# Kernel tuning notes

Measured on AMD Instinct MI355X. Metric: run time of the kernel, lower is better.

Reference implementation:

```python
import jax, jax.numpy as jnp
import numpy as np

N_NODES = 50000
N_EDGES = 800000
HID = 128


def setup_inputs() -> dict:
    key = jax.random.key(0)
    ks = jax.random.split(key, 10)
    s_msg = 1.0 / np.sqrt(2 * HID + 1)
    s_u1 = 1.0 / np.sqrt(2 * HID)
    s_u2 = 1.0 / np.sqrt(HID)
    return {
        "z": jax.random.normal(ks[0], (N_NODES, HID), dtype=jnp.float32),
        "edge_weight": jax.random.uniform(ks[1], (N_EDGES,), dtype=jnp.float32),
        "edge_src": jax.random.randint(ks[2], (N_EDGES,), 0, N_NODES),
        "edge_dst": jax.random.randint(ks[3], (N_EDGES,), 0, N_NODES),
        "Wm": jax.random.normal(ks[4], (2 * HID + 1, HID), dtype=jnp.float32) * s_msg,
        "bm": jax.random.normal(ks[5], (HID,), dtype=jnp.float32) * s_msg,
        "W1": jax.random.normal(ks[6], (2 * HID, HID), dtype=jnp.float32) * s_u1,
        "b1": jax.random.normal(ks[7], (HID,), dtype=jnp.float32) * s_u1,
        "W2": jax.random.normal(ks[8], (HID, HID), dtype=jnp.float32) * s_u2,
        "b2": jax.random.normal(ks[9], (HID,), dtype=jnp.float32) * s_u2,
    }


def reference(z, edge_weight, edge_src, edge_dst, Wm, bm, W1, b1, W2, b2):
    n, H = z.shape
    # message Linear on concat([z[u], z[v], w]) split to avoid materializing [E, 2H+1]
    Wd, Ws, ww = Wm[:H], Wm[H:2 * H], Wm[2 * H]  # [H,H], [H,H], [H]
    msgs = (z[edge_dst] @ Wd + z[edge_src] @ Ws
            + edge_weight[:, None] * ww[None, :] + bm)  # [E, H]
    # max-aggregate messages per destination node; zeros for isolated nodes
    agg = jax.ops.segment_max(msgs, edge_dst, num_segments=n)  # [n, H], -inf if empty
    deg = jax.ops.segment_sum(jnp.ones_like(edge_weight), edge_dst, num_segments=n)
    agg = jnp.where(deg[:, None] > 0, agg, jnp.zeros((), dtype=z.dtype))
    # update MLP on concat([z, agg]) split into two GEMMs
    W1a, W1b = W1[:H], W1[H:]
    hidden = jax.nn.relu(z @ W1a + agg @ W1b + b1)  # [n, H]
    return hidden @ W2 + b2  # [n, H]
```

## Files before the change

kernel.cpp:

```cpp
#include <hip/hip_runtime.h>
#include <hip/hip_bf16.h>

#define HID 128

typedef short bf16x8 __attribute__((ext_vector_type(8)));
typedef float f32x4  __attribute__((ext_vector_type(4)));
typedef unsigned short u16;
typedef unsigned long long u64;

__device__ __forceinline__ u16 f2bf(float f) {
    __hip_bfloat16 h = __float2bfloat16(f);
    return *reinterpret_cast<u16*>(&h);
}
__device__ __forceinline__ float bf2f(u16 x) {
    unsigned u = ((unsigned)x) << 16;
    return __uint_as_float(u);
}
__device__ __forceinline__ u64 pack_rec(int dst, int src, float w) {
    int wq = (int)fmaf(w, 32768.f, 0.5f);
    wq = wq > 32767 ? 32767 : wq;
    return ((u64)(unsigned)dst << 31) | ((unsigned)src << 15) | (unsigned)wq;
}


__global__ __launch_bounds__(256)
void hist_kernel(const int* __restrict__ edst, int* __restrict__ bhist,
                 int E, int nbk)
{
    __shared__ int lh[256];
    const int b = blockIdx.x;
    const int t = threadIdx.x;
    lh[t] = 0;
    __syncthreads();
    const int e0 = b * 4096;
    const int eend = min(e0 + 4096, E);
    for (int e = e0 + t; e < eend; e += 256)
        atomicAdd(&lh[edst[e] >> 8], 1);
    __syncthreads();
    if (t < nbk && lh[t] > 0) atomicAdd(&bhist[t], lh[t]);
}

__global__ __launch_bounds__(256)
void cast_scatter(const float* __restrict__ z, const float* __restrict__ Wm,
                  const float* __restrict__ W1, const float* __restrict__ W2,
                  const int* __restrict__ esrc, const int* __restrict__ edst,
                  const float* __restrict__ ew,
                  const int* __restrict__ bhist, int* __restrict__ brun,
                  u16* __restrict__ Ab, u16* __restrict__ Wt, u64* __restrict__ tmp,
                  int N, int Mp, int E, int bz, int bw, int nbk)
{
    const int b = blockIdx.x;
    const int t = threadIdx.x;
    if (b < bz) {
        const int idx8 = (b * 256 + t) * 8;
        const int row = idx8 >> 7, col = idx8 & 127;
        bf16x8 u;
        if (row < N) {
            const float4 v0 = *(const float4*)&z[(size_t)row * 128 + col];
            const float4 v1 = *(const float4*)&z[(size_t)row * 128 + col + 4];
            u[0] = (short)f2bf(v0.x); u[1] = (short)f2bf(v0.y);
            u[2] = (short)f2bf(v0.z); u[3] = (short)f2bf(v0.w);
            u[4] = (short)f2bf(v1.x); u[5] = (short)f2bf(v1.y);
            u[6] = (short)f2bf(v1.z); u[7] = (short)f2bf(v1.w);
        } else { u = bf16x8{0,0,0,0,0,0,0,0}; }
        *(bf16x8*)&Ab[(size_t)row * 256 + col] = u;
    } else if (b < bz + bw) {
        const int idx = (b - bz) * 256 + t;
        float v;
        if (idx < 32768) {
            const int nn = idx >> 7, k = idx & 127;
            v = (nn < 128) ? Wm[k * 128 + nn] : Wm[(128 + k) * 128 + (nn - 128)];
        } else if (idx < 65536) {
            const int j = idx - 32768, n = j >> 8, k = j & 255;
            v = W1[k * 128 + n];
        } else {
            const int j = idx - 65536, n = j >> 7, k = j & 127;
            v = W2[k * 128 + n];
        }
        Wt[idx] = f2bf(v);
    } else {
        __shared__ int cnt[256];
        __shared__ int rbase[256];
        __shared__ int bbase[256];
        __shared__ int ps[256];
        const int e0 = (b - bz - bw) * 4096;
        const int eend = min(e0 + 4096, E);

        const int h = (t < nbk) ? bhist[t] : 0;
        ps[t] = h;
        __syncthreads();
        for (int off = 1; off < 256; off <<= 1) {
            int add = (t >= off) ? ps[t - off] : 0;
            __syncthreads();
            ps[t] += add;
            __syncthreads();
        }
        bbase[t] = ps[t] - h;
        cnt[t] = 0;
        __syncthreads();

        if (eend - e0 == 4096) {
            int myb[16]; u64 myrec[16];
#pragma unroll
            for (int i = 0; i < 16; i++) {
                const int e = e0 + t + i * 256;
                const int d = edst[e];
                myb[i] = d >> 8;
                myrec[i] = pack_rec(d, esrc[e], ew[e]);
                atomicAdd(&cnt[myb[i]], 1);
            }
            __syncthreads();
            if (t < nbk && cnt[t] > 0) rbase[t] = bbase[t] + atomicAdd(&brun[t], cnt[t]);
            __syncthreads();
            cnt[t] = 0;
            __syncthreads();
#pragma unroll
            for (int i = 0; i < 16; i++) {
                const int r = atomicAdd(&cnt[myb[i]], 1);
                tmp[(size_t)rbase[myb[i]] + r] = myrec[i];
            }
        } else {
            for (int e = e0 + t; e < eend; e += 256)
                atomicAdd(&cnt[edst[e] >> 8], 1);
            __syncthreads();
            if (t < nbk && cnt[t] > 0) rbase[t] = bbase[t] + atomicAdd(&brun[t], cnt[t]);
            __syncthreads();
            cnt[t] = 0;
            __syncthreads();
            for (int e = e0 + t; e < eend; e += 256) {
                const int d = edst[e];
                const int bk = d >> 8;
                const int r = atomicAdd(&cnt[bk], 1);
                tmp[(size_t)rbase[bk] + r] = pack_rec(d, esrc[e], ew[e]);
            }
        }
    }
}

__global__ __launch_bounds__(256)
void sort_gemmP(const u64* __restrict__ tmp, const int* __restrict__ bhist,
                int* __restrict__ offsets, unsigned* __restrict__ s_ew,
                int N, int E, int nbk,
                const u16* __restrict__ Ab, const u16* __restrict__ Wt,
                u16* __restrict__ Pb, int Mp, int nP,
                const float* __restrict__ Wm, const float* __restrict__ b1,
                const float* __restrict__ bm,
                u16* __restrict__ W1f, float* __restrict__ bprime)
{
    const int t = threadIdx.x;

    if (blockIdx.x < (unsigned)nbk) {
        __shared__ int cnt[256];
        __shared__ int cur[256];
        __shared__ int ps[256];
        const int b = blockIdx.x;
        const int n0 = b << 8;
        const int nhi = min(256, N - n0);

        const int h = (t < nbk) ? bhist[t] : 0;
        ps[t] = h;
        __syncthreads();
        for (int off = 1; off < 256; off <<= 1) {
            int add = (t >= off) ? ps[t - off] : 0;
            __syncthreads();
            ps[t] += add;
            __syncthreads();
        }
        const int base = (b > 0) ? ps[b - 1] : 0;
        const int endp = ps[b];
        cnt[t] = 0;
        __syncthreads();

        for (int r = base + t; r < endp; r += 256)
            atomicAdd(&cnt[(int)(tmp[r] >> 31) - n0], 1);
        __syncthreads();

        const int v = cnt[t];
        ps[t] = v;
        __syncthreads();
        for (int off = 1; off < 256; off <<= 1) {
            int add = (t >= off) ? ps[t - off] : 0;
            __syncthreads();
            ps[t] += add;
            __syncthreads();
        }
        cur[t] = base + ps[t] - v;
        __syncthreads();

        if (t < nhi) offsets[n0 + t] = cur[t];
        if (t == 0 && n0 + nhi == N) offsets[N] = E;

        for (int r = base + t; r < endp; r += 256) {
            const u64 rec = tmp[r];
            const int local = (int)(rec >> 31) - n0;
            const int pos = atomicAdd(&cur[local], 1);
            s_ew[pos] = (unsigned)(rec & 0x7FFFFFFFu);
        }
    } else if (blockIdx.x < (unsigned)(nbk + nP)) {
        __shared__ u16 As[64 * 136];
        const int row0 = (blockIdx.x - nbk) * 64;
        const int wv = t >> 6, lane = t & 63;
        const int wy = wv & 1, wx = wv >> 1;
        const int q = lane >> 4, n = lane & 15;

#pragma unroll
        for (int i = 0; i < 4; i++) {
            const int chunk = i * 256 + t;
            const int row = chunk >> 4;
            const int c8 = chunk & 15;
            *(bf16x8*)&As[row * 136 + c8 * 8] =
                *(const bf16x8*)&Ab[(size_t)(row0 + row) * 256 + c8 * 8];
        }
        __syncthreads();

        const u16* pAl = As + (wy * 32 + n) * 136 + q * 8;
        const u16* pB = Wt + (size_t)(128 + wx * 64 + n) * 128 + q * 8;

        f32x4 acc[2][4];
#pragma unroll
        for (int i = 0; i < 2; i++)
#pragma unroll
            for (int j = 0; j < 4; j++) acc[i][j] = f32x4{0.f, 0.f, 0.f, 0.f};

#pragma unroll
        for (int kk = 0; kk < 128; kk += 32) {
            bf16x8 a0 = *(const bf16x8*)(pAl + kk);
            bf16x8 a1 = *(const bf16x8*)(pAl + 16 * 136 + kk);
            bf16x8 bfr[4];
#pragma unroll
            for (int ni = 0; ni < 4; ni++)
                bfr[ni] = *(const bf16x8*)(pB + (size_t)ni * 16 * 128 + kk);
#pragma unroll
            for (int ni = 0; ni < 4; ni++) {
                acc[0][ni] = __builtin_amdgcn_mfma_f32_16x16x32_bf16(a0, bfr[ni], acc[0][ni], 0, 0, 0);
                acc[1][ni] = __builtin_amdgcn_mfma_f32_16x16x32_bf16(a1, bfr[ni], acc[1][ni], 0, 0, 0);
            }
        }

#pragma unroll
        for (int mi = 0; mi < 2; mi++) {
#pragma unroll
            for (int ni = 0; ni < 4; ni++) {
                const int rbase2 = row0 + wy * 32 + mi * 16 + q * 4;
                const int c = wx * 64 + ni * 16 + n;
#pragma unroll
                for (int r = 0; r < 4; r++)
                    Pb[(size_t)(rbase2 + r) * 128 + c] = f2bf(acc[mi][ni][r]);
            }
        }
    } else {
        const u16* W1t = Wt + 32768;
        const int wv = t >> 6, lane = t & 63;
        const int q = lane >> 4, n16 = lane & 15;

#pragma unroll
        for (int i = 0; i < 8; i++) {
            const int idx8 = (i * 256 + t) * 8;
            const int row = idx8 >> 7, c = idx8 & 127;
            *(bf16x8*)&W1f[row * 256 + 128 + c] =
                *(const bf16x8*)&W1t[row * 256 + 128 + c];
        }

        const int r0 = wv * 32;
        const u16* pA = W1t + (size_t)(r0 + n16) * 256 + 128 + q * 8;

        f32x4 acc[2][8];
#pragma unroll
        for (int i = 0; i < 2; i++)
#pragma unroll
            for (int j = 0; j < 8; j++) acc[i][j] = f32x4{0.f, 0.f, 0.f, 0.f};

#pragma unroll
        for (int kk = 0; kk < 128; kk += 32) {
            bf16x8 a0 = *(const bf16x8*)(pA + kk);
            bf16x8 a1 = *(const bf16x8*)(pA + 16 * 256 + kk);
            bf16x8 bfr[8];
#pragma unroll
            for (int ni = 0; ni < 8; ni++) {
                const float* src = &Wm[(size_t)(ni * 16 + n16) * 128 + kk + q * 8];
                const float4 v0 = *(const float4*)src;
                const float4 v1 = *(const float4*)(src + 4);
                bf16x8 bb;
                bb[0] = (short)f2bf(v0.x); bb[1] = (short)f2bf(v0.y);
                bb[2] = (short)f2bf(v0.z); bb[3] = (short)f2bf(v0.w);
                bb[4] = (short)f2bf(v1.x); bb[5] = (short)f2bf(v1.y);
                bb[6] = (short)f2bf(v1.z); bb[7] = (short)f2bf(v1.w);
                bfr[ni] = bb;
            }
#pragma unroll
            for (int ni = 0; ni < 8; ni++) {
                acc[0][ni] = __builtin_amdgcn_mfma_f32_16x16x32_bf16(a0, bfr[ni], acc[0][ni], 0, 0, 0);
                acc[1][ni] = __builtin_amdgcn_mfma_f32_16x16x32_bf16(a1, bfr[ni], acc[1][ni], 0, 0, 0);
            }
        }

#pragma unroll
        for (int mi = 0; mi < 2; mi++) {
#pragma unroll
            for (int ni = 0; ni < 8; ni++) {
                const int row = r0 + mi * 16 + q * 4;
                const int c = ni * 16 + n16;
#pragma unroll
                for (int r = 0; r < 4; r++) {
                    const int rr = row + r;
                    W1f[rr * 256 + c] =
                        f2bf(acc[mi][ni][r] + bf2f(W1t[rr * 256 + c]));
                }
            }
        }

        if (t < 128) {
            float s = b1[t];
            for (int c = 0; c < 128; c++)
                s = fmaf(bm[c], bf2f(W1t[t * 256 + 128 + c]), s);
            bprime[t] = s;
        }
    }
}

__global__ __launch_bounds__(256)
void aggregate_kernel(const u16* __restrict__ Pb,
                      const float* __restrict__ bm,
                      const float* __restrict__ ww,
                      const int* __restrict__ offsets,
                      const unsigned* __restrict__ s_ew,
                      u16* __restrict__ Ab,
                      const u16* __restrict__ WdT,
                      int N, int Mp)
{
    const int t = threadIdx.x;
    const int lane = t & 63;
    const int c0 = (lane & 15) * 8;
    const int nd = blockIdx.x * 16 + ((t >> 6) << 2) + (lane >> 4);
    if (nd >= Mp) return;

    u16* dst = &Ab[(size_t)nd * 256 + 128 + c0];

    if (nd >= N) {
        bf16x8 zv = {0, 0, 0, 0, 0, 0, 0, 0};
        *(bf16x8*)dst = zv;
        return;
    }

    const int start = offsets[nd];
    const int end   = offsets[nd + 1];

    if (end <= start) {
        float acc8[8];
#pragma unroll
        for (int j = 0; j < 8; j++) acc8[j] = 0.f;
        for (int k = 0; k < 128; k++) {
            const float zk = bf2f(Ab[(size_t)nd * 256 + k]);
#pragma unroll
            for (int j = 0; j < 8; j++)
                acc8[j] = fmaf(zk, bf2f(WdT[(size_t)(c0 + j) * 128 + k]), acc8[j]);
        }
        bf16x8 outv;
#pragma unroll
        for (int j = 0; j < 8; j++)
            outv[j] = (short)f2bf(-(acc8[j] + bm[c0 + j]));
        *(bf16x8*)dst = outv;
        return;
    }

    float wwv[8];
    {
        const float4 wa = *(const float4*)&ww[c0];
        const float4 wb = *(const float4*)&ww[c0 + 4];
        wwv[0] = wa.x; wwv[1] = wa.y; wwv[2] = wa.z; wwv[3] = wa.w;
        wwv[4] = wb.x; wwv[5] = wb.y; wwv[6] = wb.z; wwv[7] = wb.w;
    }

    const float kq = 1.f / 32768.f;
    float m[8];
#pragma unroll
    for (int j = 0; j < 8; j++) m[j] = -INFINITY;

    const int last = end - 1;
    for (int eb = start; eb < end; eb += 8) {
        unsigned u[8];
#pragma unroll
        for (int i = 0; i < 8; i++) {
            int e = eb + i; if (e > last) e = last;
            u[i] = s_ew[e];
        }
        bf16x8 p[8];
#pragma unroll
        for (int i = 0; i < 8; i++)
            p[i] = *(const bf16x8*)&Pb[(size_t)(u[i] >> 15) * 128 + c0];
#pragma unroll
        for (int i = 0; i < 8; i++) {
            const float w = (float)(u[i] & 32767u) * kq;
#pragma unroll
            for (int j = 0; j < 8; j++)
                m[j] = fmaxf(m[j], fmaf(w, wwv[j], bf2f((u16)p[i][j])));
        }
    }

    bf16x8 outv;
#pragma unroll
    for (int j = 0; j < 8; j++)
        outv[j] = (short)f2bf(m[j]);
    *(bf16x8*)dst = outv;
}

__global__ __launch_bounds__(256)
void gemm_HO(const u16* __restrict__ Ab, const u16* __restrict__ W1t,
             const float* __restrict__ b1, const u16* __restrict__ W2t,
             const float* __restrict__ b2, float* __restrict__ out, int Mstore)
{
    __shared__ u16 smem[64 * 264];

    const int row0 = blockIdx.x * 64;
    const int tid = threadIdx.x;
    const int wv = tid >> 6, lane = tid & 63;
    const int wy = wv & 1, wx = wv >> 1;
    const int q = lane >> 4, n = lane & 15;

#pragma unroll
    for (int i = 0; i < 8; i++) {
        const int chunk = i * 256 + tid;
        const int row = chunk >> 5;
        const int c8 = chunk & 31;
        *(bf16x8*)&smem[row * 264 + c8 * 8] =
            *(const bf16x8*)&Ab[(size_t)(row0 + row) * 256 + c8 * 8];
    }
    __syncthreads();

    f32x4 acc[2][4];

    {
        const u16* pAl = smem + (wy * 32 + n) * 264 + q * 8;
        const u16* pB = W1t + (size_t)(wx * 64 + n) * 256 + q * 8;

#pragma unroll
        for (int i = 0; i < 2; i++)
#pragma unroll
            for (int j = 0; j < 4; j++) acc[i][j] = f32x4{0.f, 0.f, 0.f, 0.f};

#pragma unroll
        for (int kk = 0; kk < 256; kk += 32) {
            bf16x8 b0 = *(const bf16x8*)(pB + kk);
            bf16x8 b1f = *(const bf16x8*)(pB + 16 * 256 + kk);
            bf16x8 b2f = *(const bf16x8*)(pB + 32 * 256 + kk);
            bf16x8 b3f = *(const bf16x8*)(pB + 48 * 256 + kk);
            bf16x8 a0 = *(const bf16x8*)(pAl + kk);
            bf16x8 a1 = *(const bf16x8*)(pAl + 16 * 264 + kk);
            acc[0][0] = __builtin_amdgcn_mfma_f32_16x16x32_bf16(a0, b0,  acc[0][0], 0, 0, 0);
            acc[0][1] = __builtin_amdgcn_mfma_f32_16x16x32_bf16(a0, b1f, acc[0][1], 0, 0, 0);
            acc[0][2] = __builtin_amdgcn_mfma_f32_16x16x32_bf16(a0, b2f, acc[0][2], 0, 0, 0);
            acc[0][3] = __builtin_amdgcn_mfma_f32_16x16x32_bf16(a0, b3f, acc[0][3], 0, 0, 0);
            acc[1][0] = __builtin_amdgcn_mfma_f32_16x16x32_bf16(a1, b0,  acc[1][0], 0, 0, 0);
            acc[1][1] = __builtin_amdgcn_mfma_f32_16x16x32_bf16(a1, b1f, acc[1][1], 0, 0, 0);
            acc[1][2] = __builtin_amdgcn_mfma_f32_16x16x32_bf16(a1, b2f, acc[1][2], 0, 0, 0);
            acc[1][3] = __builtin_amdgcn_mfma_f32_16x16x32_bf16(a1, b3f, acc[1][3], 0, 0, 0);
        }
    }
    __syncthreads();

#pragma unroll
    for (int mi = 0; mi < 2; mi++) {
#pragma unroll
        for (int ni = 0; ni < 4; ni++) {
            const int rl = wy * 32 + mi * 16 + q * 4;
            const int c = wx * 64 + ni * 16 + n;
#pragma unroll
            for (int r = 0; r < 4; r++) {
                float v = acc[mi][ni][r] + b1[c];
                smem[(rl + r) * 136 + c] = f2bf(fmaxf(v, 0.f));
            }
        }
    }
    __syncthreads();

    {
        const u16* pB = W2t + (size_t)(wx * 64 + n) * 128 + q * 8;
        const u16* pHl = smem + (wy * 32 + n) * 136 + q * 8;

#pragma unroll
        for (int i = 0; i < 2; i++)
#pragma unroll
            for (int j = 0; j < 4; j++) acc[i][j] = f32x4{0.f, 0.f, 0.f, 0.f};

#pragma unroll
        for (int kk = 0; kk < 128; kk += 32) {
            bf16x8 b0 = *(const bf16x8*)(pB + kk);
            bf16x8 b1f = *(const bf16x8*)(pB + 16 * 128 + kk);
            bf16x8 b2f = *(const bf16x8*)(pB + 32 * 128 + kk);
            bf16x8 b3f = *(const bf16x8*)(pB + 48 * 128 + kk);
            bf16x8 a0 = *(const bf16x8*)(pHl + kk);
            bf16x8 a1 = *(const bf16x8*)(pHl + 16 * 136 + kk);
            acc[0][0] = __builtin_amdgcn_mfma_f32_16x16x32_bf16(a0, b0,  acc[0][0], 0, 0, 0);
            acc[0][1] = __builtin_amdgcn_mfma_f32_16x16x32_bf16(a0, b1f, acc[0][1], 0, 0, 0);
            acc[0][2] = __builtin_amdgcn_mfma_f32_16x16x32_bf16(a0, b2f, acc[0][2], 0, 0, 0);
            acc[0][3] = __builtin_amdgcn_mfma_f32_16x16x32_bf16(a0, b3f, acc[0][3], 0, 0, 0);
            acc[1][0] = __builtin_amdgcn_mfma_f32_16x16x32_bf16(a1, b0,  acc[1][0], 0, 0, 0);
            acc[1][1] = __builtin_amdgcn_mfma_f32_16x16x32_bf16(a1, b1f, acc[1][1], 0, 0, 0);
            acc[1][2] = __builtin_amdgcn_mfma_f32_16x16x32_bf16(a1, b2f, acc[1][2], 0, 0, 0);
            acc[1][3] = __builtin_amdgcn_mfma_f32_16x16x32_bf16(a1, b3f, acc[1][3], 0, 0, 0);
        }

#pragma unroll
        for (int mi = 0; mi < 2; mi++) {
#pragma unroll
            for (int ni = 0; ni < 4; ni++) {
                const int rbase = row0 + wy * 32 + mi * 16 + q * 4;
                const int c = wx * 64 + ni * 16 + n;
#pragma unroll
                for (int r = 0; r < 4; r++) {
                    const int rr = rbase + r;
                    if (rr >= Mstore) continue;
                    out[(size_t)rr * 128 + c] = acc[mi][ni][r] + b2[c];
                }
            }
        }
    }
}

extern "C" void kernel_launch(void* const* d_in, const int* in_sizes, int n_in,
                              void* d_out, int out_size, void* d_ws, size_t ws_size,
                              hipStream_t stream) {
    const float* z    = (const float*)d_in[0];
    const float* ew   = (const float*)d_in[1];
    const int*   esrc = (const int*)d_in[2];
    const int*   edst = (const int*)d_in[3];
    const float* Wm   = (const float*)d_in[4];
    const float* bm   = (const float*)d_in[5];
    const float* W1   = (const float*)d_in[6];
    const float* b1   = (const float*)d_in[7];
    const float* W2   = (const float*)d_in[8];
    const float* b2   = (const float*)d_in[9];
    float* out = (float*)d_out;

    const int N  = in_sizes[0] / HID;
    const int E  = in_sizes[1];
    const int Mp = ((N + 63) / 64) * 64;
    const int nbk = (N + 255) / 256;
    const int nP  = Mp / 64;

    char* w = (char*)d_ws;
    u16*  Ab      = (u16*)w;      w += (size_t)Mp * 256 * 2;
    u16*  Pb      = (u16*)w;      w += (size_t)Mp * 128 * 2;
    u16*  Wt      = (u16*)w;      w += (size_t)81920 * 2;
    u16*  W1f     = (u16*)w;      w += (size_t)32768 * 2;
    float* bprime = (float*)w;    w += 128 * 4;
    int*  offsets = (int*)w;      w += (size_t)(N + 64) * 4;
    int*  bhist   = (int*)w;      w += 256 * 4;
    int*  brun    = (int*)w;      w += 256 * 4;
    unsigned* s_ew = (unsigned*)w; w += (size_t)E * 4;
    u64*  tmp     = (u64*)w;      w += (size_t)E * 8;

    const int bz8 = (Mp * 16 + 255) / 256;
    const int bw  = (81920 + 255) / 256;
    const int nsc = (E + 4095) / 4096;

    hipMemsetAsync(bhist, 0, 512 * sizeof(int), stream);
    hist_kernel<<<nsc, 256, 0, stream>>>(edst, bhist, E, nbk);
    cast_scatter<<<bz8 + bw + nsc, 256, 0, stream>>>(z, Wm, W1, W2, esrc, edst, ew,
                                                     bhist, brun, Ab, Wt, tmp,
                                                     N, Mp, E, bz8, bw, nbk);
    sort_gemmP<<<nbk + nP + 1, 256, 0, stream>>>(tmp, bhist, offsets, s_ew,
                                                 N, E, nbk, Ab, Wt, Pb, Mp, nP,
                                                 Wm, b1, bm, W1f, bprime);
    aggregate_kernel<<<(Mp + 15) / 16, 256, 0, stream>>>(Pb, bm, Wm + 256 * 128,
                                                         offsets, s_ew, Ab, Wt,
                                                         N, Mp);
    gemm_HO<<<Mp / 64, 256, 0, stream>>>(Ab, W1f, bprime, Wt + 65536, b2, out, N);
}
```

Baseline: 204.8 us.

## Replace two-pass bucket sort with per-node degree counting sort via global atomics

The edge CSR build no longer runs a bucketed two-pass sort through a 64-bit temp array. It now counts per-node degree with global atomics during the prep pass and scans those counts into offsets. A scatter pass then places 32-bit records using per-node atomic cursors, and the P GEMM runs alongside it. This drops the hist kernel, the 8-byte temp round trip and the second local sort, at the cost of heavy contended global atomics on deg and woff.

```diff
diff --git a/kernel.cpp b/kernel.cpp
--- a/kernel.cpp
+++ b/kernel.cpp
@@ -16,38 +16,20 @@
     unsigned u = ((unsigned)x) << 16;
     return __uint_as_float(u);
 }
-__device__ __forceinline__ u64 pack_rec(int dst, int src, float w) {
+__device__ __forceinline__ unsigned pack_sw(int src, float w) {
     int wq = (int)fmaf(w, 32768.f, 0.5f);
     wq = wq > 32767 ? 32767 : wq;
-    return ((u64)(unsigned)dst << 31) | ((unsigned)src << 15) | (unsigned)wq;
+    return ((unsigned)src << 15) | (unsigned)wq;
 }
 
 
 __global__ __launch_bounds__(256)
-void hist_kernel(const int* __restrict__ edst, int* __restrict__ bhist,
-                 int E, int nbk)
-{
-    __shared__ int lh[256];
-    const int b = blockIdx.x;
-    const int t = threadIdx.x;
-    lh[t] = 0;
-    __syncthreads();
-    const int e0 = b * 4096;
-    const int eend = min(e0 + 4096, E);
-    for (int e = e0 + t; e < eend; e += 256)
-        atomicAdd(&lh[edst[e] >> 8], 1);
-    __syncthreads();
-    if (t < nbk && lh[t] > 0) atomicAdd(&bhist[t], lh[t]);
-}
-
-__global__ __launch_bounds__(256)
-void cast_scatter(const float* __restrict__ z, const float* __restrict__ Wm,
-                  const float* __restrict__ W1, const float* __restrict__ W2,
-                  const int* __restrict__ esrc, const int* __restrict__ edst,
-                  const float* __restrict__ ew,
-                  const int* __restrict__ bhist, int* __restrict__ brun,
-                  u16* __restrict__ Ab, u16* __restrict__ Wt, u64* __restrict__ tmp,
-                  int N, int Mp, int E, int bz, int bw, int nbk)
+void prep(const float* __restrict__ z, const float* __restrict__ Wm,
+          const float* __restrict__ W1, const float* __restrict__ W2,
+          const int* __restrict__ edst,
+          u16* __restrict__ Ab, u16* __restrict__ Wt,
+          int* __restrict__ deg, int* __restrict__ bhist,
+          int N, int Mp, int E, int bz, int bw, int nbk)
 {
     const int b = blockIdx.x;
     const int t = threadIdx.x;
@@ -79,12 +61,37 @@
         }
         Wt[idx] = f2bf(v);
     } else {
-        __shared__ int cnt[256];
-        __shared__ int rbase[256];
-        __shared__ int bbase[256];
-        __shared__ int ps[256];
+        __shared__ int lh[256];
+        lh[t] = 0;
+        __syncthreads();
         const int e0 = (b - bz - bw) * 4096;
         const int eend = min(e0 + 4096, E);
+        for (int e = e0 + t; e < eend; e += 256) {
+            const int d = edst[e];
+            atomicAdd(&lh[d >> 8], 1);
+            atomicAdd(&deg[d], 1);
+        }
+        __syncthreads();
+        if (t < nbk && lh[t] > 0) atomicAdd(&bhist[t], lh[t]);
+    }
+}
+
+__global__ __launch_bounds__(256)
+void scan_fold(const int* __restrict__ deg, const int* __restrict__ bhist,
+               int* __restrict__ offsets, int* __restrict__ woff,
+               int N, int E, int nbk,
+               const u16* __restrict__ Wt, const float* __restrict__ Wm,
+               const float* __restrict__ b1, const float* __restrict__ bm,
+               u16* __restrict__ W1f, float* __restrict__ bprime)
+{
+    const int t = threadIdx.x;
+
+    if (blockIdx.x < (unsigned)nbk) {
+        __shared__ int ps[256];
+        __shared__ int ns[256];
+        const int b = blockIdx.x;
+        const int n0 = b << 8;
+        const int nhi = min(256, N - n0);
 
         const int h = (t < nbk) ? bhist[t] : 0;
         ps[t] = h;
@@ -95,159 +102,20 @@
             ps[t] += add;
             __syncthreads();
         }
-        bbase[t] = ps[t] - h;
-        cnt[t] = 0;
-        __syncthreads();
-
-        if (eend - e0 == 4096) {
-            int myb[16]; u64 myrec[16];
-#pragma unroll
-            for (int i = 0; i < 16; i++) {
-                const int e = e0 + t + i * 256;
-                const int d = edst[e];
-                myb[i] = d >> 8;
-                myrec[i] = pack_rec(d, esrc[e], ew[e]);
-                atomicAdd(&cnt[myb[i]], 1);
-            }
-            __syncthreads();
-            if (t < nbk && cnt[t] > 0) rbase[t] = bbase[t] + atomicAdd(&brun[t], cnt[t]);
-            __syncthreads();
-            cnt[t] = 0;
-            __syncthreads();
-#pragma unroll
-            for (int i = 0; i < 16; i++) {
-                const int r = atomicAdd(&cnt[myb[i]], 1);
-                tmp[(size_t)rbase[myb[i]] + r] = myrec[i];
-            }
-        } else {
-            for (int e = e0 + t; e < eend; e += 256)
-                atomicAdd(&cnt[edst[e] >> 8], 1);
-            __syncthreads();
-            if (t < nbk && cnt[t] > 0) rbase[t] = bbase[t] + atomicAdd(&brun[t], cnt[t]);
-            __syncthreads();
-            cnt[t] = 0;
-            __syncthreads();
-            for (int e = e0 + t; e < eend; e += 256) {
-                const int d = edst[e];
-                const int bk = d >> 8;
-                const int r = atomicAdd(&cnt[bk], 1);
-                tmp[(size_t)rbase[bk] + r] = pack_rec(d, esrc[e], ew[e]);
-            }
-        }
-    }
-}
-
-__global__ __launch_bounds__(256)
-void sort_gemmP(const u64* __restrict__ tmp, const int* __restrict__ bhist,
-                int* __restrict__ offsets, unsigned* __restrict__ s_ew,
-                int N, int E, int nbk,
-                const u16* __restrict__ Ab, const u16* __restrict__ Wt,
-                u16* __restrict__ Pb, int Mp, int nP,
-                const float* __restrict__ Wm, const float* __restrict__ b1,
-                const float* __restrict__ bm,
-                u16* __restrict__ W1f, float* __restrict__ bprime)
-{
-    const int t = threadIdx.x;
-
-    if (blockIdx.x < (unsigned)nbk) {
-        __shared__ int cnt[256];
-        __shared__ int cur[256];
-        __shared__ int ps[256];
-        const int b = blockIdx.x;
-        const int n0 = b << 8;
-        const int nhi = min(256, N - n0);
-
-        const int h = (t < nbk) ? bhist[t] : 0;
-        ps[t] = h;
+        const int base = (b > 0) ? ps[b - 1] : 0;
+
+        const int dv = (t < nhi) ? deg[n0 + t] : 0;
+        ns[t] = dv;
         __syncthreads();
         for (int off = 1; off < 256; off <<= 1) {
-            int add = (t >= off) ? ps[t - off] : 0;
+            int add = (t >= off) ? ns[t - off] : 0;
             __syncthreads();
-            ps[t] += add;
+            ns[t] += add;
             __syncthreads();
         }
-        const int base = (b > 0) ? ps[b - 1] : 0;
-        const int endp = ps[b];
-        cnt[t] = 0;
-        __syncthreads();
-
-        for (int r = base + t; r < endp; r += 256)
-            atomicAdd(&cnt[(int)(tmp[r] >> 31) - n0], 1);
-        __syncthreads();
-
-        const int v = cnt[t];
-        ps[t] = v;
-        __syncthreads();
-        for (int off = 1; off < 256; off <<= 1) {
-            int add = (t >= off) ? ps[t - off] : 0;
-            __syncthreads();
-            ps[t] += add;
-            __syncthreads();
-        }
-        cur[t] = base + ps[t] - v;
-        __syncthreads();
-
-        if (t < nhi) offsets[n0 + t] = cur[t];
-        if (t == 0 && n0 + nhi == N) offsets[N] = E;
-
-        for (int r = base + t; r < endp; r += 256) {
-            const u64 rec = tmp[r];
-            const int local = (int)(rec >> 31) - n0;
-            const int pos = atomicAdd(&cur[local], 1);
-            s_ew[pos] = (unsigned)(rec & 0x7FFFFFFFu);
-        }
-    } else if (blockIdx.x < (unsigned)(nbk + nP)) {
-        __shared__ u16 As[64 * 136];
-        const int row0 = (blockIdx.x - nbk) * 64;
-        const int wv = t >> 6, lane = t & 63;
-        const int wy = wv & 1, wx = wv >> 1;
-        const int q = lane >> 4, n = lane & 15;
-
-#pragma unroll
-        for (int i = 0; i < 4; i++) {
-            const int chunk = i * 256 + t;
-            const int row = chunk >> 4;
-            const int c8 = chunk & 15;
-            *(bf16x8*)&As[row * 136 + c8 * 8] =
-                *(const bf16x8*)&Ab[(size_t)(row0 + row) * 256 + c8 * 8];
-        }
-        __syncthreads();
-
-        const u16* pAl = As + (wy * 32 + n) * 136 + q * 8;
-        const u16* pB = Wt + (size_t)(128 + wx * 64 + n) * 128 + q * 8;
-
-        f32x4 acc[2][4];
-#pragma unroll
-        for (int i = 0; i < 2; i++)
-#pragma unroll
-            for (int j = 0; j < 4; j++) acc[i][j] = f32x4{0.f, 0.f, 0.f, 0.f};
-
-#pragma unroll
-        for (int kk = 0; kk < 128; kk += 32) {
-            bf16x8 a0 = *(const bf16x8*)(pAl + kk);
-            bf16x8 a1 = *(const bf16x8*)(pAl + 16 * 136 + kk);
-            bf16x8 bfr[4];
-#pragma unroll
-            for (int ni = 0; ni < 4; ni++)
-                bfr[ni] = *(const bf16x8*)(pB + (size_t)ni * 16 * 128 + kk);
-#pragma unroll
-            for (int ni = 0; ni < 4; ni++) {
-                acc[0][ni] = __builtin_amdgcn_mfma_f32_16x16x32_bf16(a0, bfr[ni], acc[0][ni], 0, 0, 0);
-                acc[1][ni] = __builtin_amdgcn_mfma_f32_16x16x32_bf16(a1, bfr[ni], acc[1][ni], 0, 0, 0);
-            }
-        }
-
-#pragma unroll
-        for (int mi = 0; mi < 2; mi++) {
-#pragma unroll
-            for (int ni = 0; ni < 4; ni++) {
-                const int rbase2 = row0 + wy * 32 + mi * 16 + q * 4;
-                const int c = wx * 64 + ni * 16 + n;
-#pragma unroll
-                for (int r = 0; r < 4; r++)
-                    Pb[(size_t)(rbase2 + r) * 128 + c] = f2bf(acc[mi][ni][r]);
-            }
-        }
+        const int o = base + ns[t] - dv;
+        if (t < nhi) { offsets[n0 + t] = o; woff[n0 + t] = o; }
+        if (b == nbk - 1 && t == 0) offsets[N] = E;
     } else {
         const u16* W1t = Wt + 32768;
         const int wv = t >> 6, lane = t & 63;
@@ -314,6 +182,93 @@
             for (int c = 0; c < 128; c++)
                 s = fmaf(bm[c], bf2f(W1t[t * 256 + 128 + c]), s);
             bprime[t] = s;
+        }
+    }
+}
+
+__global__ __launch_bounds__(256)
+void scatter_gemmP(const int* __restrict__ esrc, const int* __restrict__ edst,
+                   const float* __restrict__ ew,
+                   int* __restrict__ woff, unsigned* __restrict__ s_ew,
+                   int E, int nsc,
+                   const u16* __restrict__ Ab, const u16* __restrict__ Wt,
+                   u16* __restrict__ Pb)
+{
+    const int t = threadIdx.x;
+
+    if (blockIdx.x < (unsigned)nsc) {
+        const int e0 = blockIdx.x * 4096;
+        const int eend = min(e0 + 4096, E);
+        if (eend - e0 == 4096) {
+            int d[16]; unsigned rec[16];
+#pragma unroll
+            for (int i = 0; i < 16; i++) {
+                const int e = e0 + t + i * 256;
+                d[i] = edst[e];
+                rec[i] = pack_sw(esrc[e], ew[e]);
+            }
+#pragma unroll
+            for (int i = 0; i < 16; i++) {
+                const int pos = atomicAdd(&woff[d[i]], 1);
+                s_ew[pos] = rec[i];
+            }
+        } else {
+            for (int e = e0 + t; e < eend; e += 256) {
+                const int pos = atomicAdd(&woff[edst[e]], 1);
+                s_ew[pos] = pack_sw(esrc[e], ew[e]);
+            }
+        }
+    } else {
+        __shared__ u16 As[64 * 136];
+        const int row0 = (blockIdx.x - nsc) * 64;
+        const int wv = t >> 6, lane = t & 63;
+        const int wy = wv & 1, wx = wv >> 1;
+        const int q = lane >> 4, n = lane & 15;
+
+#pragma unroll
+        for (int i = 0; i < 4; i++) {
+            const int chunk = i * 256 + t;
+            const int row = chunk >> 4;
+            const int c8 = chunk & 15;
+            *(bf16x8*)&As[row * 136 + c8 * 8] =
+                *(const bf16x8*)&Ab[(size_t)(row0 + row) * 256 + c8 * 8];
+        }
+        __syncthreads();
+
+        const u16* pAl = As + (wy * 32 + n) * 136 + q * 8;
+        const u16* pB = Wt + (size_t)(128 + wx * 64 + n) * 128 + q * 8;
+
+        f32x4 acc[2][4];
+#pragma unroll
+        for (int i = 0; i < 2; i++)
+#pragma unroll
+            for (int j = 0; j < 4; j++) acc[i][j] = f32x4{0.f, 0.f, 0.f, 0.f};
+
+#pragma unroll
+        for (int kk = 0; kk < 128; kk += 32) {
+            bf16x8 a0 = *(const bf16x8*)(pAl + kk);
+            bf16x8 a1 = *(const bf16x8*)(pAl + 16 * 136 + kk);
+            bf16x8 bfr[4];
+#pragma unroll
+            for (int ni = 0; ni < 4; ni++)
+                bfr[ni] = *(const bf16x8*)(pB + (size_t)ni * 16 * 128 + kk);
+#pragma unroll
+            for (int ni = 0; ni < 4; ni++) {
+                acc[0][ni] = __builtin_amdgcn_mfma_f32_16x16x32_bf16(a0, bfr[ni], acc[0][ni], 0, 0, 0);
+                acc[1][ni] = __builtin_amdgcn_mfma_f32_16x16x32_bf16(a1, bfr[ni], acc[1][ni], 0, 0, 0);
+            }
+        }
+
+#pragma unroll
+        for (int mi = 0; mi < 2; mi++) {
+#pragma unroll
+            for (int ni = 0; ni < 4; ni++) {
+                const int rbase2 = row0 + wy * 32 + mi * 16 + q * 4;
+                const int c = wx * 64 + ni * 16 + n;
+#pragma unroll
+                for (int r = 0; r < 4; r++)
+                    Pb[(size_t)(rbase2 + r) * 128 + c] = f2bf(acc[mi][ni][r]);
+            }
         }
     }
 }
@@ -545,23 +500,22 @@
     u16*  W1f     = (u16*)w;      w += (size_t)32768 * 2;
     float* bprime = (float*)w;    w += 128 * 4;
     int*  offsets = (int*)w;      w += (size_t)(N + 64) * 4;
+    int*  woff    = (int*)w;      w += (size_t)(N + 64) * 4;
+    int*  deg     = (int*)w;      w += (size_t)(N + 64) * 4;
     int*  bhist   = (int*)w;      w += 256 * 4;
-    int*  brun    = (int*)w;      w += 256 * 4;
     unsigned* s_ew = (unsigned*)w; w += (size_t)E * 4;
-    u64*  tmp     = (u64*)w;      w += (size_t)E * 8;
 
     const int bz8 = (Mp * 16 + 255) / 256;
     const int bw  = (81920 + 255) / 256;
     const int nsc = (E + 4095) / 4096;
 
-    hipMemsetAsync(bhist, 0, 512 * sizeof(int), stream);
-    hist_kernel<<<nsc, 256, 0, stream>>>(edst, bhist, E, nbk);
-    cast_scatter<<<bz8 + bw + nsc, 256, 0, stream>>>(z, Wm, W1, W2, esrc, edst, ew,
-                                                     bhist, brun, Ab, Wt, tmp,
-                                                     N, Mp, E, bz8, bw, nbk);
-    sort_gemmP<<<nbk + nP + 1, 256, 0, stream>>>(tmp, bhist, offsets, s_ew,
-                                                 N, E, nbk, Ab, Wt, Pb, Mp, nP,
-                                                 Wm, b1, bm, W1f, bprime);
+    hipMemsetAsync(deg, 0, ((size_t)(N + 64) + 256) * sizeof(int), stream);
+    prep<<<bz8 + bw + nsc, 256, 0, stream>>>(z, Wm, W1, W2, edst, Ab, Wt,
+                                             deg, bhist, N, Mp, E, bz8, bw, nbk);
+    scan_fold<<<nbk + 1, 256, 0, stream>>>(deg, bhist, offsets, woff, N, E, nbk,
+                                           Wt, Wm, b1, bm, W1f, bprime);
+    scatter_gemmP<<<nsc + nP, 256, 0, stream>>>(esrc, edst, ew, woff, s_ew, E, nsc,
+                                                Ab, Wt, Pb);
     aggregate_kernel<<<(Mp + 15) / 16, 256, 0, stream>>>(Pb, bm, Wm + 256 * 128,
                                                          offsets, s_ew, Ab, Wt,
                                                          N, Mp);
```

After: 258.4 us. 26.2% more time.
